# Kernel tuning notes

Measured on AMD Instinct MI355X. Metric: run time of the kernel, lower is better.

The kernel has to match this reference:

```python
import jax, jax.numpy as jnp
import numpy as np

B, L = 128, 256
VOCAB, E, PF = 50000, 300, 50
C, K, R = 512, 3, 53
D3 = (E + 2 * PF) * 3  # 1200, conv input channels


def setup_inputs() -> dict:
    key = jax.random.key(0)
    ks = jax.random.split(key, 12)
    return {
        "context": jax.random.randint(ks[0], (B, L), 0, VOCAB),
        "subject_idx": jnp.sort(jax.random.randint(ks[1], (B, 2), 0, L), axis=-1),
        "object_idx": jnp.sort(jax.random.randint(ks[2], (B, 2), 0, L), axis=-1),
        "subject_dis": jax.random.randint(ks[3], (B, L), 0, 2 * L),
        "object_dis": jax.random.randint(ks[4], (B, L), 0, 2 * L),
        "embed_table": jax.random.normal(ks[5], (VOCAB, E), dtype=jnp.float32),
        "pos_table": jax.random.normal(ks[6], (2 * L, PF), dtype=jnp.float32),
        "conv_w": jax.random.normal(ks[7], (C, D3, K), dtype=jnp.float32) * (1.0 / np.sqrt(D3 * K)),
        "conv_b": jax.random.normal(ks[8], (C,), dtype=jnp.float32) * 0.01,
        "rela_linear_w": jax.random.normal(ks[9], (R, C), dtype=jnp.float32) * (1.0 / np.sqrt(C)),
        "rela_emb": jax.random.normal(ks[10], (R, C), dtype=jnp.float32),
    }


def _span_mean(wf3, idx):
    # mean of wf3[b, start:end+1, :] per sample, vectorized with a mask
    pos = jnp.arange(wf3.shape[1])[None, :]
    m = ((pos >= idx[:, 0:1]) & (pos <= idx[:, 1:2])).astype(wf3.dtype)  # B,L
    return jnp.einsum("bld,bl->bd", wf3, m) / jnp.sum(m, axis=1, keepdims=True)


def reference(context, subject_idx, object_idx, subject_dis, object_dis,
              embed_table, pos_table, conv_w, conv_b, rela_linear_w, rela_emb):
    emb = embed_table[context]                                            # B,L,E
    posf = jnp.concatenate([pos_table[subject_dis], pos_table[object_dis]], axis=2)
    wf = jnp.concatenate([emb, posf], axis=2)                             # B,L,D
    wp = jnp.pad(wf, ((0, 0), (1, 1), (0, 0)))
    # sliding window concat of [i-1, i, i+1]
    wf3 = jnp.concatenate([wp[:, :-2], wp[:, 1:-1], wp[:, 2:]], axis=2)   # B,L,3D

    subj = _span_mean(wf3, subject_idx)                                   # B,3D
    obj = _span_mean(wf3, object_idx)
    rs = jax.nn.softmax(jnp.einsum("bld,bd->bl", wf3, subj), axis=1)
    ro = jax.nn.softmax(jnp.einsum("bld,bd->bl", wf3, obj), axis=1)
    wf3 = wf3 * ((rs + ro) * 0.5)[:, :, None]

    x = jnp.transpose(wf3, (0, 2, 1))                                     # B,3D,L
    y = jax.lax.conv_general_dilated(x, conv_w, (1,), [(K // 2, K // 2)],
                                     dimension_numbers=("NCH", "OIH", "NCH"))
    sent = jnp.transpose(jnp.tanh(y + conv_b[None, :, None]), (0, 2, 1))  # B,L,C

    attn = jnp.einsum("blr,rc->blc",
                      jnp.einsum("blc,rc->blr", sent, rela_linear_w), rela_emb)
    attn = jax.nn.softmax(attn, axis=1)  # softmax over sequence positions
    wo = jnp.max(sent * attn, axis=1)                                     # B,C
    wo = wo / jnp.maximum(jnp.linalg.norm(wo, axis=1, keepdims=True), 1e-12)
    all_dist = jnp.linalg.norm(wo[:, None, :] - rela_emb[None, :, :], axis=2)  # B,R
    return all_dist
```

## Files before the change

### kernel.cpp

```cpp
#include <hip/hip_runtime.h>
#include <hip/hip_bf16.h>
#include <math.h>

#define B_  128
#define L_  256
#define E_  300
#define PF_ 50
#define D_  400
#define D3_ 1200
#define C_  512
#define KW_ 3
#define R_  53
#define M_  (B_*L_)
#define KP_ 1216
#define K3_ (3*KP_)
#define LROWS_ 258

typedef __attribute__((ext_vector_type(8))) short bf16x8;
typedef __attribute__((ext_vector_type(8))) unsigned short u16x8;
typedef __attribute__((ext_vector_type(4))) float f32x4;

__device__ __forceinline__ unsigned short f2bf(float f) {
    union { float f; unsigned u; } x; x.f = f;
    unsigned r = x.u + 0x7FFF + ((x.u >> 16) & 1);
    return (unsigned short)(r >> 16);
}
__device__ __forceinline__ float bf2f(unsigned short u) {
    union { unsigned u; float f; } x; x.u = ((unsigned)u) << 16;
    return x.f;
}

__device__ __forceinline__ void gld16(const void* g, void* l) {
    __builtin_amdgcn_global_load_lds(
        (const __attribute__((address_space(1))) void*)g,
        (__attribute__((address_space(3))) void*)l, 16, 0, 0);
}

__global__ void prep_kernel(const float* __restrict__ conv_w, const float* __restrict__ rlw,
                            const float* __restrict__ re, unsigned short* __restrict__ WpT,
                            unsigned short* __restrict__ MmatT) {
    int idx = blockIdx.x * blockDim.x + threadIdx.x;
    if (idx < C_ * K3_) {
        int c = idx / K3_, q = idx % K3_;
        int k = q / KP_, ch = q % KP_;
        WpT[idx] = (ch < D3_) ? f2bf(conv_w[c * (D3_ * KW_) + ch * KW_ + k]) : (unsigned short)0;
    } else {
        int j = idx - C_ * K3_;
        if (j >= C_ * C_) return;
        int n = j / C_, k = j % C_;
        float acc = 0.f;
        for (int r = 0; r < R_; ++r)
            acc += rlw[r * C_ + k] * re[r * C_ + n];
        MmatT[j] = f2bf(acc);
    }
}

__global__ void build_wf_kernel(const int* __restrict__ ctx, const int* __restrict__ sdis,
                                const int* __restrict__ odis, const float* __restrict__ emb,
                                const float* __restrict__ pos, float* __restrict__ wf) {
    const int total = M_ * D_;
    for (int idx = blockIdx.x * blockDim.x + threadIdx.x; idx < total;
         idx += gridDim.x * blockDim.x) {
        int d = idx % D_;
        int bt = idx / D_;
        float v;
        if (d < E_)            v = emb[(long)ctx[bt] * E_ + d];
        else if (d < E_ + PF_) v = pos[sdis[bt] * PF_ + (d - E_)];
        else                   v = pos[odis[bt] * PF_ + (d - E_ - PF_)];
        wf[idx] = v;
    }
}

__global__ __launch_bounds__(512) void span_sum_kernel(
    const float* __restrict__ wf, const int* __restrict__ sidx, const int* __restrict__ oidx,
    float* __restrict__ SS, float* __restrict__ OS) {
    const int b = blockIdx.x, e = blockIdx.y;
    const int* idx = e ? oidx : sidx;
    float* out = e ? OS : SS;
    const int s0 = idx[b * 2], s1 = idx[b * 2 + 1];
    const float inv = 1.f / (float)(s1 - s0 + 1);
    const int d = threadIdx.x;
    if (d >= D_) return;

    const float* base_p = wf + (size_t)(b << 8) * D_ + d;
    float base = 0.f;
    for (int t = s0; t <= s1; ++t) base += base_p[(size_t)t * D_];

    float w_s0 = base_p[(size_t)s0 * D_];
    float w_s1 = base_p[(size_t)s1 * D_];
    float j0 = base - w_s1 + ((s0 > 0) ? base_p[(size_t)(s0 - 1) * D_] : 0.f);
    float j2 = base - w_s0 + ((s1 < L_ - 1) ? base_p[(size_t)(s1 + 1) * D_] : 0.f);

    out[((size_t)(b * 3 + 0)) * D_ + d] = j0 * inv;
    out[((size_t)(b * 3 + 1)) * D_ + d] = base * inv;
    out[((size_t)(b * 3 + 2)) * D_ + d] = j2 * inv;
}

__global__ __launch_bounds__(256) void dots_kernel(
    const float* __restrict__ wf, const float* __restrict__ SS, const float* __restrict__ OS,
    float* __restrict__ dsb, float* __restrict__ ddb) {
    const int wave = threadIdx.x >> 6, lane = threadIdx.x & 63;
    const int g = blockIdx.x * 4 + wave;
    const int b = g >> 8, t = g & 255;
    float ds = 0.f, dd = 0.f;
#pragma unroll
    for (int j = 0; j < 3; ++j) {
        int u = t + j - 1;
        if ((unsigned)u < (unsigned)L_) {
            const float4* w  = (const float4*)(wf + ((size_t)((b << 8) + u)) * D_);
            const float4* ss = (const float4*)(SS + ((size_t)(b * 3 + j)) * D_);
            const float4* oo = (const float4*)(OS + ((size_t)(b * 3 + j)) * D_);
            for (int q = lane; q < D_ / 4; q += 64) {
                float4 wv = w[q], sv = ss[q], ov = oo[q];
                ds += wv.x * sv.x + wv.y * sv.y + wv.z * sv.z + wv.w * sv.w;
                dd += wv.x * ov.x + wv.y * ov.y + wv.z * ov.z + wv.w * ov.w;
            }
        }
    }
#pragma unroll
    for (int off = 32; off > 0; off >>= 1) {
        ds += __shfl_down(ds, off);
        dd += __shfl_down(dd, off);
    }
    if (lane == 0) { dsb[g] = ds; ddb[g] = dd; }
}

__global__ __launch_bounds__(256) void softmax_s_kernel(
    const float* __restrict__ dsb, const float* __restrict__ ddb, float* __restrict__ s) {
    const int b = blockIdx.x, tid = threadIdx.x;
    __shared__ float red[256];
    float ds = dsb[(b << 8) + tid];
    float dd = ddb[(b << 8) + tid];

    red[tid] = ds; __syncthreads();
    for (int st = 128; st > 0; st >>= 1) {
        if (tid < st) red[tid] = fmaxf(red[tid], red[tid + st]);
        __syncthreads();
    }
    float ms = red[0]; __syncthreads();
    float es = expf(ds - ms);
    red[tid] = es; __syncthreads();
    for (int st = 128; st > 0; st >>= 1) {
        if (tid < st) red[tid] += red[tid + st];
        __syncthreads();
    }
    float zs = red[0]; __syncthreads();

    red[tid] = dd; __syncthreads();
    for (int st = 128; st > 0; st >>= 1) {
        if (tid < st) red[tid] = fmaxf(red[tid], red[tid + st]);
        __syncthreads();
    }
    float mo = red[0]; __syncthreads();
    float eo = expf(dd - mo);
    red[tid] = eo; __syncthreads();
    for (int st = 128; st > 0; st >>= 1) {
        if (tid < st) red[tid] += red[tid + st];
        __syncthreads();
    }
    float zo = red[0];

    s[(b << 8) + tid] = 0.5f * (es / zs + eo / zo);
}

__global__ void build_xsp_kernel(const float* __restrict__ wf, const float* __restrict__ s,
                                 unsigned short* __restrict__ XSp) {
    const int CH8 = KP_ / 8;
    int idx = blockIdx.x * blockDim.x + threadIdx.x;
    const int total = B_ * LROWS_ * CH8;
    if (idx >= total) return;
    int chunk = idx % CH8;
    int rb = idx / CH8;
    int row = rb % LROWS_;
    int b = rb / LROWS_;

    u16x8 out = {0,0,0,0,0,0,0,0};
    int t = row - 1;
    int ch0 = chunk * 8;
    if ((unsigned)t < (unsigned)L_ && ch0 < D3_) {
        int j = ch0 / D_;
        int d0 = ch0 - j * D_;
        int u = t + j - 1;
        if ((unsigned)u < (unsigned)L_) {
            float sc = s[(b << 8) + t];
            const float* w = wf + ((size_t)((b << 8) + u)) * D_ + d0;
#pragma unroll
            for (int q = 0; q < 8; ++q) out[q] = f2bf(sc * w[q]);
        }
    }
    *(u16x8*)&XSp[((size_t)(b * LROWS_ + row)) * KP_ + ch0] = out;
}

template<int MODE>
__global__ __launch_bounds__(512, 2) void gemm8_kernel(
    const unsigned short* __restrict__ Aglob, const unsigned short* __restrict__ Bglob,
    const float* __restrict__ conv_b, unsigned short* __restrict__ outb) {
    extern __shared__ unsigned short lds[];
    const int tid = threadIdx.x;
    const int lane = tid & 63;
    const int wave = tid >> 6;
    const int wr = wave >> 2;
    const int wc = wave & 3;
    const int bx = blockIdx.x;
    const int blockN = blockIdx.y * 256;
    const int l15 = lane & 15;
    const int NT = (MODE == 0) ? (K3_ / 64) : (C_ / 64);
    const size_t Astr = (MODE == 0) ? (size_t)KP_ : (size_t)C_;
    const size_t Bstr = (MODE == 0) ? (size_t)K3_ : (size_t)C_;

    const int arole = wc;
    const int bhalf = wc >> 1;
    const int brole = wr * 2 + (wc & 1);

    const int acol0 = (((lane >> 4) + 0) ^ (l15 & 7)) * 8;
    const int acol1 = (((lane >> 4) + 4) ^ (l15 & 7)) * 8;
    const int bro = (wc & 1) * 64;

    auto stageA = [&](int kt, int buf) {
        const unsigned short* gb;
        if constexpr (MODE == 0) {
            int tap = kt / KP_, ch0 = kt - tap * KP_;
            gb = Aglob + ((size_t)(bx * LROWS_ + wr * 128 + tap)) * KP_ + ch0;
        } else {
            gb = Aglob + ((size_t)(bx * 256 + wr * 128)) * C_ + kt;
        }
        unsigned short* pb = &lds[(buf * 2 + wr) * 8192];
#pragma unroll
        for (int i = 0; i < 4; ++i) {
            int sl = arole * 256 + i * 64 + lane;
            int row = sl >> 3, p = sl & 7;
            int colg = p ^ (row & 7);
            gld16(gb + (size_t)row * Astr + colg * 8, (char*)pb + sl * 16);
        }
    };
    auto stageB = [&](int kt, int buf) {
        const unsigned short* gb = Bglob + ((size_t)(blockN + bhalf * 128)) * Bstr + kt;
        unsigned short* pb = &lds[32768 + (buf * 2 + bhalf) * 8192];
#pragma unroll
        for (int i = 0; i < 4; ++i) {
            int sl = brole * 256 + i * 64 + lane;
            int row = sl >> 3, p = sl & 7;
            int colg = p ^ (row & 7);
            gld16(gb + (size_t)row * Bstr + colg * 8, (char*)pb + sl * 16);
        }
    };

    f32x4 acc[8][4] = {};

    stageA(0, 0);
    stageB(0, 0);
    __syncthreads();

    int cur = 0;
    for (int kt = 0; kt < NT * 64; kt += 64, cur ^= 1) {
        int ktn = kt + 64;
        if (ktn >= NT * 64) ktn = 0;
        const unsigned short* Ap = &lds[(cur * 2 + wr) * 8192];
        const unsigned short* Bp = &lds[32768 + (cur * 2 + bhalf) * 8192];

        bf16x8 a[8], b0, b1;

#pragma unroll
        for (int mi = 0; mi < 8; ++mi) a[mi] = *(const bf16x8*)&Ap[(mi * 16 + l15) * 64 + acol0];
        b0 = *(const bf16x8*)&Bp[(bro + 0 * 16 + l15) * 64 + acol0];
        b1 = *(const bf16x8*)&Bp[(bro + 1 * 16 + l15) * 64 + acol0];
        stageA(ktn, cur ^ 1);
        __builtin_amdgcn_s_setprio(1);
#pragma unroll
        for (int mi = 0; mi < 8; ++mi) {
            acc[mi][0] = __builtin_amdgcn_mfma_f32_16x16x32_bf16(a[mi], b0, acc[mi][0], 0, 0, 0);
            acc[mi][1] = __builtin_amdgcn_mfma_f32_16x16x32_bf16(a[mi], b1, acc[mi][1], 0, 0, 0);
        }
        __builtin_amdgcn_s_setprio(0);

        b0 = *(const bf16x8*)&Bp[(bro + 2 * 16 + l15) * 64 + acol0];
        b1 = *(const bf16x8*)&Bp[(bro + 3 * 16 + l15) * 64 + acol0];
        stageB(ktn, cur ^ 1);
        __builtin_amdgcn_s_setprio(1);
#pragma unroll
        for (int mi = 0; mi < 8; ++mi) {
            acc[mi][2] = __builtin_amdgcn_mfma_f32_16x16x32_bf16(a[mi], b0, acc[mi][2], 0, 0, 0);
            acc[mi][3] = __builtin_amdgcn_mfma_f32_16x16x32_bf16(a[mi], b1, acc[mi][3], 0, 0, 0);
        }
        __builtin_amdgcn_s_setprio(0);

#pragma unroll
        for (int mi = 0; mi < 8; ++mi) a[mi] = *(const bf16x8*)&Ap[(mi * 16 + l15) * 64 + acol1];
        b0 = *(const bf16x8*)&Bp[(bro + 0 * 16 + l15) * 64 + acol1];
        b1 = *(const bf16x8*)&Bp[(bro + 1 * 16 + l15) * 64 + acol1];
        __builtin_amdgcn_s_setprio(1);
#pragma unroll
        for (int mi = 0; mi < 8; ++mi) {
            acc[mi][0] = __builtin_amdgcn_mfma_f32_16x16x32_bf16(a[mi], b0, acc[mi][0], 0, 0, 0);
            acc[mi][1] = __builtin_amdgcn_mfma_f32_16x16x32_bf16(a[mi], b1, acc[mi][1], 0, 0, 0);
        }
        __builtin_amdgcn_s_setprio(0);

        b0 = *(const bf16x8*)&Bp[(bro + 2 * 16 + l15) * 64 + acol1];
        b1 = *(const bf16x8*)&Bp[(bro + 3 * 16 + l15) * 64 + acol1];
        __builtin_amdgcn_s_setprio(1);
#pragma unroll
        for (int mi = 0; mi < 8; ++mi) {
            acc[mi][2] = __builtin_amdgcn_mfma_f32_16x16x32_bf16(a[mi], b0, acc[mi][2], 0, 0, 0);
            acc[mi][3] = __builtin_amdgcn_mfma_f32_16x16x32_bf16(a[mi], b1, acc[mi][3], 0, 0, 0);
        }
        __builtin_amdgcn_s_setprio(0);

        __syncthreads();
    }

    const int r4 = ((lane >> 4) << 2);
#pragma unroll
    for (int mi = 0; mi < 8; ++mi) {
#pragma unroll
        for (int nj = 0; nj < 4; ++nj) {
            const int col = blockN + wc * 64 + nj * 16 + l15;
            const int row0 = bx * 256 + wr * 128 + mi * 16 + r4;
            if constexpr (MODE == 0) {
                float bias = conv_b[col];
#pragma unroll
                for (int r = 0; r < 4; ++r)
                    outb[(size_t)(row0 + r) * C_ + col] = f2bf(tanhf(acc[mi][nj][r] + bias));
            } else {
#pragma unroll
                for (int r = 0; r < 4; ++r)
                    outb[(size_t)(row0 + r) * C_ + col] = f2bf(acc[mi][nj][r]);
            }
        }
    }
}

__global__ __launch_bounds__(256) void softmax_wo_kernel(
    const unsigned short* __restrict__ P, const unsigned short* __restrict__ sent,
    float* __restrict__ wo) {
    const int b = blockIdx.x;
    const int c = blockIdx.y * 256 + threadIdx.x;
    const unsigned short* Pb = P + ((size_t)(b << 8)) * C_ + c;
    const unsigned short* Sb = sent + ((size_t)(b << 8)) * C_ + c;
    float m = bf2f(Pb[0]);
    float z = 1.f;
    float wm = bf2f(Sb[0]);
    for (int l = 1; l < L_; ++l) {
        float p = bf2f(Pb[(size_t)l * C_]);
        float sv = bf2f(Sb[(size_t)l * C_]);
        if (p <= m) {
            float e = expf(p - m);
            z += e;
            wm = fmaxf(wm, sv * e);
        } else {
            float sc = expf(m - p);
            z = z * sc + 1.f;
            wm = fmaxf(wm * sc, sv);
            m = p;
        }
    }
    wo[b * C_ + c] = wm / z;
}

__global__ __launch_bounds__(256) void final_kernel(
    const float* __restrict__ wo, const float* __restrict__ re, float* __restrict__ out) {
    const int b = blockIdx.x, tid = threadIdx.x;
    __shared__ float won[C_];
    __shared__ float red[256];
    float p = 0.f;
    for (int c = tid; c < C_; c += 256) {
        float v = wo[b * C_ + c];
        p += v * v;
    }
    red[tid] = p; __syncthreads();
    for (int st = 128; st > 0; st >>= 1) {
        if (tid < st) red[tid] += red[tid + st];
        __syncthreads();
    }
    float inv = 1.f / fmaxf(sqrtf(red[0]), 1e-12f);
    for (int c = tid; c < C_; c += 256) won[c] = wo[b * C_ + c] * inv;
    __syncthreads();
    const int wv = tid >> 6, lane = tid & 63;
    for (int r = wv; r < R_; r += 4) {
        float acc2 = 0.f;
        for (int c = lane; c < C_; c += 64) {
            float dlt = won[c] - re[r * C_ + c];
            acc2 += dlt * dlt;
        }
        for (int off = 32; off > 0; off >>= 1) acc2 += __shfl_down(acc2, off);
        if (lane == 0) out[b * R_ + r] = sqrtf(acc2);
    }
}

extern "C" void kernel_launch(void* const* d_in, const int* in_sizes, int n_in,
                              void* d_out, int out_size, void* d_ws, size_t ws_size,
                              hipStream_t stream) {
    const int* context     = (const int*)d_in[0];
    const int* subject_idx = (const int*)d_in[1];
    const int* object_idx  = (const int*)d_in[2];
    const int* subject_dis = (const int*)d_in[3];
    const int* object_dis  = (const int*)d_in[4];
    const float* embed_table = (const float*)d_in[5];
    const float* pos_table   = (const float*)d_in[6];
    const float* conv_w      = (const float*)d_in[7];
    const float* conv_b      = (const float*)d_in[8];
    const float* rlw         = (const float*)d_in[9];
    const float* re          = (const float*)d_in[10];
    float* out = (float*)d_out;

    char* ws = (char*)d_ws;
    size_t off = 0;
    auto alloc = [&](size_t bytes) {
        void* p = ws + off;
        off = (off + bytes + 255) & ~(size_t)255;
        return p;
    };
    float* wf            = (float*)alloc((size_t)M_ * D_ * 4);
    float* s             = (float*)alloc((size_t)M_ * 4);
    unsigned short* XSp  = (unsigned short*)alloc((size_t)B_ * LROWS_ * KP_ * 2);
    unsigned short* WpT  = (unsigned short*)alloc((size_t)C_ * K3_ * 2);
    unsigned short* MmatT= (unsigned short*)alloc((size_t)C_ * C_ * 2);
    unsigned short* sent = (unsigned short*)alloc((size_t)M_ * C_ * 2);
    float* wo            = (float*)alloc((size_t)B_ * C_ * 4);
    float* SS            = (float*)alloc((size_t)B_ * 3 * D_ * 4);
    float* OS            = (float*)alloc((size_t)B_ * 3 * D_ * 4);
    float* dsb           = (float*)alloc((size_t)M_ * 4);
    float* ddb           = (float*)alloc((size_t)M_ * 4);
    unsigned short* P = XSp;

    (void)hipFuncSetAttribute((const void*)gemm8_kernel<0>,
                              hipFuncAttributeMaxDynamicSharedMemorySize, 131072);
    (void)hipFuncSetAttribute((const void*)gemm8_kernel<1>,
                              hipFuncAttributeMaxDynamicSharedMemorySize, 131072);

    prep_kernel<<<(C_ * K3_ + C_ * C_ + 255) / 256, 256, 0, stream>>>(
        conv_w, rlw, re, WpT, MmatT);
    build_wf_kernel<<<4096, 256, 0, stream>>>(context, subject_dis, object_dis,
                                              embed_table, pos_table, wf);
    span_sum_kernel<<<dim3(B_, 2), 512, 0, stream>>>(wf, subject_idx, object_idx, SS, OS);
    dots_kernel<<<M_ / 4, 256, 0, stream>>>(wf, SS, OS, dsb, ddb);
    softmax_s_kernel<<<B_, 256, 0, stream>>>(dsb, ddb, s);
    build_xsp_kernel<<<(B_ * LROWS_ * (KP_ / 8) + 255) / 256, 256, 0, stream>>>(wf, s, XSp);
    gemm8_kernel<0><<<dim3(M_ / 256, C_ / 256), 512, 131072, stream>>>(
        XSp, WpT, conv_b, sent);
    gemm8_kernel<1><<<dim3(M_ / 256, C_ / 256), 512, 131072, stream>>>(
        sent, MmatT, nullptr, P);
    softmax_wo_kernel<<<dim3(B_, 2), 256, 0, stream>>>(P, sent, wo);
    final_kernel<<<B_, 256, 0, stream>>>(wo, re, out);
}
```

Before: 375.8 us.

## Split conv GEMM into smaller-tile kernel with swizzled block order

```diff
diff --git a/kernel.cpp b/kernel.cpp
--- a/kernel.cpp
+++ b/kernel.cpp
@@ -191,10 +191,94 @@
     *(u16x8*)&XSp[((size_t)(b * LROWS_ + row)) * KP_ + ch0] = out;
 }
 
-template<int MODE>
-__global__ __launch_bounds__(512, 2) void gemm8_kernel(
-    const unsigned short* __restrict__ Aglob, const unsigned short* __restrict__ Bglob,
-    const float* __restrict__ conv_b, unsigned short* __restrict__ outb) {
+__global__ __launch_bounds__(256) void conv4_kernel(
+    const unsigned short* __restrict__ XSp, const unsigned short* __restrict__ WpT,
+    const float* __restrict__ conv_b, unsigned short* __restrict__ sent) {
+    extern __shared__ unsigned short lds[];
+    const int tid = threadIdx.x;
+    const int lane = tid & 63;
+    const int wave = tid >> 6;
+    const int wr = wave >> 1, wc = wave & 1;
+    const int lin = blockIdx.x;
+    const int bx = ((lin & 7) << 5) | (lin >> 5);
+    const int by = (lin >> 3) & 3;
+    const int l15 = lane & 15;
+    const int acol0 = (((lane >> 4) + 0) ^ (l15 & 7)) * 8;
+    const int acol1 = (((lane >> 4) + 4) ^ (l15 & 7)) * 8;
+    const int NT = K3_ / 64;
+
+    const int xrow0 = (bx >> 1) * LROWS_ + (bx & 1) * 128;
+
+    auto stage = [&](int kt, int buf) {
+        int tap = kt / KP_, ch0 = kt - tap * KP_;
+        const unsigned short* ga = XSp + ((size_t)(xrow0 + tap)) * KP_ + ch0;
+        const unsigned short* gb = WpT + ((size_t)(by * 128)) * K3_ + kt;
+        unsigned short* pa = &lds[buf * 8192];
+        unsigned short* pb = &lds[16384 + buf * 8192];
+#pragma unroll
+        for (int i = 0; i < 4; ++i) {
+            int sl = i * 256 + tid;
+            int row = sl >> 3, p = sl & 7;
+            int colg = p ^ (row & 7);
+            gld16(ga + (size_t)row * KP_ + colg * 8, (char*)pa + sl * 16);
+            gld16(gb + (size_t)row * K3_ + colg * 8, (char*)pb + sl * 16);
+        }
+    };
+
+    f32x4 acc[4][4] = {};
+
+    stage(0, 0);
+    __syncthreads();
+
+    int cur = 0;
+    for (int kt = 0; kt < NT * 64; kt += 64, cur ^= 1) {
+        int ktn = kt + 64;
+        if (ktn >= NT * 64) ktn = 0;
+        const unsigned short* Ap = &lds[cur * 8192];
+        const unsigned short* Bp = &lds[16384 + cur * 8192];
+
+        bf16x8 a0[4], b0[4], a1[4], b1[4];
+#pragma unroll
+        for (int i = 0; i < 4; ++i) {
+            a0[i] = *(const bf16x8*)&Ap[(wr * 64 + i * 16 + l15) * 64 + acol0];
+            b0[i] = *(const bf16x8*)&Bp[(wc * 64 + i * 16 + l15) * 64 + acol0];
+            a1[i] = *(const bf16x8*)&Ap[(wr * 64 + i * 16 + l15) * 64 + acol1];
+            b1[i] = *(const bf16x8*)&Bp[(wc * 64 + i * 16 + l15) * 64 + acol1];
+        }
+        stage(ktn, cur ^ 1);
+        __builtin_amdgcn_s_setprio(1);
+#pragma unroll
+        for (int i = 0; i < 4; ++i)
+#pragma unroll
+            for (int j = 0; j < 4; ++j)
+                acc[i][j] = __builtin_amdgcn_mfma_f32_16x16x32_bf16(a0[i], b0[j], acc[i][j], 0, 0, 0);
+#pragma unroll
+        for (int i = 0; i < 4; ++i)
+#pragma unroll
+            for (int j = 0; j < 4; ++j)
+                acc[i][j] = __builtin_amdgcn_mfma_f32_16x16x32_bf16(a1[i], b1[j], acc[i][j], 0, 0, 0);
+        __builtin_amdgcn_s_setprio(0);
+        __syncthreads();
+    }
+
+    const int r4 = ((lane >> 4) << 2);
+#pragma unroll
+    for (int mi = 0; mi < 4; ++mi) {
+#pragma unroll
+        for (int nj = 0; nj < 4; ++nj) {
+            const int col = by * 128 + wc * 64 + nj * 16 + l15;
+            const int row0 = bx * 128 + wr * 64 + mi * 16 + r4;
+            float bias = conv_b[col];
+#pragma unroll
+            for (int r = 0; r < 4; ++r)
+                sent[(size_t)(row0 + r) * C_ + col] = f2bf(tanhf(acc[mi][nj][r] + bias));
+        }
+    }
+}
+
+__global__ __launch_bounds__(512, 2) void pgemm_kernel(
+    const unsigned short* __restrict__ sent, const unsigned short* __restrict__ MmatT,
+    unsigned short* __restrict__ P) {
     extern __shared__ unsigned short lds[];
     const int tid = threadIdx.x;
     const int lane = tid & 63;
@@ -204,9 +288,7 @@
     const int bx = blockIdx.x;
     const int blockN = blockIdx.y * 256;
     const int l15 = lane & 15;
-    const int NT = (MODE == 0) ? (K3_ / 64) : (C_ / 64);
-    const size_t Astr = (MODE == 0) ? (size_t)KP_ : (size_t)C_;
-    const size_t Bstr = (MODE == 0) ? (size_t)K3_ : (size_t)C_;
+    const int NT = C_ / 64;
 
     const int arole = wc;
     const int bhalf = wc >> 1;
@@ -217,31 +299,25 @@
     const int bro = (wc & 1) * 64;
 
     auto stageA = [&](int kt, int buf) {
-        const unsigned short* gb;
-        if constexpr (MODE == 0) {
-            int tap = kt / KP_, ch0 = kt - tap * KP_;
-            gb = Aglob + ((size_t)(bx * LROWS_ + wr * 128 + tap)) * KP_ + ch0;
-        } else {
-            gb = Aglob + ((size_t)(bx * 256 + wr * 128)) * C_ + kt;
-        }
+        const unsigned short* gb = sent + ((size_t)(bx * 256 + wr * 128)) * C_ + kt;
         unsigned short* pb = &lds[(buf * 2 + wr) * 8192];
 #pragma unroll
         for (int i = 0; i < 4; ++i) {
             int sl = arole * 256 + i * 64 + lane;
             int row = sl >> 3, p = sl & 7;
             int colg = p ^ (row & 7);
-            gld16(gb + (size_t)row * Astr + colg * 8, (char*)pb + sl * 16);
+            gld16(gb + (size_t)row * C_ + colg * 8, (char*)pb + sl * 16);
         }
     };
     auto stageB = [&](int kt, int buf) {
-        const unsigned short* gb = Bglob + ((size_t)(blockN + bhalf * 128)) * Bstr + kt;
+        const unsigned short* gb = MmatT + ((size_t)(blockN + bhalf * 128)) * C_ + kt;
         unsigned short* pb = &lds[32768 + (buf * 2 + bhalf) * 8192];
 #pragma unroll
         for (int i = 0; i < 4; ++i) {
             int sl = brole * 256 + i * 64 + lane;
             int row = sl >> 3, p = sl & 7;
             int colg = p ^ (row & 7);
-            gld16(gb + (size_t)row * Bstr + colg * 8, (char*)pb + sl * 16);
+            gld16(gb + (size_t)row * C_ + colg * 8, (char*)pb + sl * 16);
         }
     };
 
@@ -316,16 +392,9 @@
         for (int nj = 0; nj < 4; ++nj) {
             const int col = blockN + wc * 64 + nj * 16 + l15;
             const int row0 = bx * 256 + wr * 128 + mi * 16 + r4;
-            if constexpr (MODE == 0) {
-                float bias = conv_b[col];
-#pragma unroll
-                for (int r = 0; r < 4; ++r)
-                    outb[(size_t)(row0 + r) * C_ + col] = f2bf(tanhf(acc[mi][nj][r] + bias));
-            } else {
-#pragma unroll
-                for (int r = 0; r < 4; ++r)
-                    outb[(size_t)(row0 + r) * C_ + col] = f2bf(acc[mi][nj][r]);
-            }
+#pragma unroll
+            for (int r = 0; r < 4; ++r)
+                P[(size_t)(row0 + r) * C_ + col] = f2bf(acc[mi][nj][r]);
         }
     }
 }
@@ -423,9 +492,9 @@
     float* ddb           = (float*)alloc((size_t)M_ * 4);
     unsigned short* P = XSp;
 
-    (void)hipFuncSetAttribute((const void*)gemm8_kernel<0>,
-                              hipFuncAttributeMaxDynamicSharedMemorySize, 131072);
-    (void)hipFuncSetAttribute((const void*)gemm8_kernel<1>,
+    (void)hipFuncSetAttribute((const void*)conv4_kernel,
+                              hipFuncAttributeMaxDynamicSharedMemorySize, 65536);
+    (void)hipFuncSetAttribute((const void*)pgemm_kernel,
                               hipFuncAttributeMaxDynamicSharedMemorySize, 131072);
 
     prep_kernel<<<(C_ * K3_ + C_ * C_ + 255) / 256, 256, 0, stream>>>(
@@ -436,10 +505,8 @@
     dots_kernel<<<M_ / 4, 256, 0, stream>>>(wf, SS, OS, dsb, ddb);
     softmax_s_kernel<<<B_, 256, 0, stream>>>(dsb, ddb, s);
     build_xsp_kernel<<<(B_ * LROWS_ * (KP_ / 8) + 255) / 256, 256, 0, stream>>>(wf, s, XSp);
-    gemm8_kernel<0><<<dim3(M_ / 256, C_ / 256), 512, 131072, stream>>>(
-        XSp, WpT, conv_b, sent);
-    gemm8_kernel<1><<<dim3(M_ / 256, C_ / 256), 512, 131072, stream>>>(
-        sent, MmatT, nullptr, P);
+    conv4_kernel<<<1024, 256, 65536, stream>>>(XSp, WpT, conv_b, sent);
+    pgemm_kernel<<<dim3(M_ / 256, C_ / 256), 512, 131072, stream>>>(sent, MmatT, P);
     softmax_wo_kernel<<<dim3(B_, 2), 256, 0, stream>>>(P, sent, wo);
     final_kernel<<<B_, 256, 0, stream>>>(wo, re, out);
 }
```

Measured after the change: 403.0 us. 1.07x slower.
